# Optimization experiments

Measured on AMD Instinct MI355X. Metric: run time of the kernel, lower is better.

## Reference

```python
import jax, jax.numpy as jnp
import numpy as np

CLASS_PERIOD = 360
MEAN = True

def setup_inputs() -> dict:
    key = jax.random.key(0)
    k1, k2 = jax.random.split(key)
    preds = jax.random.normal(k1, (131072, CLASS_PERIOD), dtype=jnp.float32)
    labels = jax.random.randint(k2, (131072,), 0, CLASS_PERIOD, dtype=jnp.int64 if jax.config.jax_enable_x64 else jnp.int32)
    return {"preds": preds, "labels": labels}

def reference(preds, labels):
    # per-row L1 normalization: x_i / sum(|x_i|)
    l1 = jnp.sum(jnp.abs(preds), axis=-1, keepdims=True)        # [B, 1]
    scaled = preds / l1                                          # [B, C]
    logp = jax.nn.log_softmax(scaled, axis=-1)                   # [B, C]
    gathered = jnp.take_along_axis(logp, labels[:, None], axis=-1)[:, 0]  # [B]
    if MEAN:
        # original: (one_hot * logp).mean() per instance = logp[label] / C
        loss = -jnp.sum(gathered) / CLASS_PERIOD
    else:
        loss = -jnp.sum(gathered)
    return loss.reshape(1)
```

## Files before the change

### kernel.cpp

```cpp
#include <hip/hip_runtime.h>
#include <hip/hip_bf16.h>
#include <math.h>

#define NROWS 131072
#define NCOLS 360
#define WAVES_PER_BLOCK 4

__global__ __launch_bounds__(256) void viewpoint_row_kernel(
    const float* __restrict__ preds,
    const int* __restrict__ labels,
    float* __restrict__ partial)
{
    const int wave = threadIdx.x >> 6;
    const int lane = threadIdx.x & 63;
    const int row  = blockIdx.x * WAVES_PER_BLOCK + wave;

    const float* p = preds + (size_t)row * NCOLS;
    const float4* p4 = (const float4*)p;

    float4 a0 = p4[lane];
    float4 a1 = make_float4(0.f, 0.f, 0.f, 0.f);
    const bool have2 = lane < (90 - 64);
    if (have2) a1 = p4[64 + lane];

    float s = fabsf(a0.x) + fabsf(a0.y) + fabsf(a0.z) + fabsf(a0.w);
    float m = fmaxf(fmaxf(a0.x, a0.y), fmaxf(a0.z, a0.w));
    if (have2) {
        s += fabsf(a1.x) + fabsf(a1.y) + fabsf(a1.z) + fabsf(a1.w);
        m = fmaxf(m, fmaxf(fmaxf(a1.x, a1.y), fmaxf(a1.z, a1.w)));
    }
    #pragma unroll
    for (int off = 32; off > 0; off >>= 1) {
        s += __shfl_xor(s, off);
        m = fmaxf(m, __shfl_xor(m, off));
    }

    const float inv = 1.0f / s;

    float e = expf((a0.x - m) * inv) + expf((a0.y - m) * inv)
            + expf((a0.z - m) * inv) + expf((a0.w - m) * inv);
    if (have2) {
        e += expf((a1.x - m) * inv) + expf((a1.y - m) * inv)
           + expf((a1.z - m) * inv) + expf((a1.w - m) * inv);
    }
    #pragma unroll
    for (int off = 32; off > 0; off >>= 1) e += __shfl_xor(e, off);

    float g = 0.f;
    if (lane == 0) {
        const int lab = labels[row];
        const float xl = p[lab];
        g = (xl - m) * inv - logf(e);
    }

    __shared__ float sh[WAVES_PER_BLOCK];
    if (lane == 0) sh[wave] = g;
    __syncthreads();
    if (threadIdx.x == 0)
        partial[blockIdx.x] = sh[0] + sh[1] + sh[2] + sh[3];
}

__global__ __launch_bounds__(256) void viewpoint_final_kernel(
    const float* __restrict__ partial, float* __restrict__ out, int n)
{
    float s = 0.f;
    for (int i = threadIdx.x; i < n; i += 256) s += partial[i];
    #pragma unroll
    for (int off = 32; off > 0; off >>= 1) s += __shfl_xor(s, off);
    __shared__ float sh[4];
    if ((threadIdx.x & 63) == 0) sh[threadIdx.x >> 6] = s;
    __syncthreads();
    if (threadIdx.x == 0)
        out[0] = -(sh[0] + sh[1] + sh[2] + sh[3]) * (1.0f / (float)NCOLS);
}

extern "C" void kernel_launch(void* const* d_in, const int* in_sizes, int n_in,
                              void* d_out, int out_size, void* d_ws, size_t ws_size,
                              hipStream_t stream) {
    const float* preds  = (const float*)d_in[0];
    const int*   labels = (const int*)d_in[1];
    float* out = (float*)d_out;
    float* partial = (float*)d_ws;

    const int nblocks = NROWS / WAVES_PER_BLOCK;
    viewpoint_row_kernel<<<nblocks, 256, 0, stream>>>(preds, labels, partial);
    viewpoint_final_kernel<<<1, 256, 0, stream>>>(partial, out, nblocks);
}
```

Before: 279.8 us.

## Process eight rows per wave, drop max pass, use fast math and shuffle gather

```diff
diff --git a/kernel.cpp b/kernel.cpp
--- a/kernel.cpp
+++ b/kernel.cpp
@@ -4,7 +4,11 @@
 
 #define NROWS 131072
 #define NCOLS 360
-#define WAVES_PER_BLOCK 4
+#define ROWS_PER_WAVE 8
+#define NWAVES (NROWS / ROWS_PER_WAVE)
+#define NBLOCKS (NWAVES / 4)
+
+typedef float f32x4 __attribute__((ext_vector_type(4)));
 
 __global__ __launch_bounds__(256) void viewpoint_row_kernel(
     const float* __restrict__ preds,
@@ -13,48 +17,49 @@
 {
     const int wave = threadIdx.x >> 6;
     const int lane = threadIdx.x & 63;
-    const int row  = blockIdx.x * WAVES_PER_BLOCK + wave;
+    const int wgid = blockIdx.x * 4 + wave;
+    const bool have2 = lane < (90 - 64);
 
-    const float* p = preds + (size_t)row * NCOLS;
-    const float4* p4 = (const float4*)p;
+    float gacc = 0.f;
 
-    float4 a0 = p4[lane];
-    float4 a1 = make_float4(0.f, 0.f, 0.f, 0.f);
-    const bool have2 = lane < (90 - 64);
-    if (have2) a1 = p4[64 + lane];
+    #pragma unroll
+    for (int r = 0; r < ROWS_PER_WAVE; ++r) {
+        const int row = r * NWAVES + wgid;
+        const f32x4* p4 = (const f32x4*)(preds + (size_t)row * NCOLS);
 
-    float s = fabsf(a0.x) + fabsf(a0.y) + fabsf(a0.z) + fabsf(a0.w);
-    float m = fmaxf(fmaxf(a0.x, a0.y), fmaxf(a0.z, a0.w));
-    if (have2) {
-        s += fabsf(a1.x) + fabsf(a1.y) + fabsf(a1.z) + fabsf(a1.w);
-        m = fmaxf(m, fmaxf(fmaxf(a1.x, a1.y), fmaxf(a1.z, a1.w)));
-    }
-    #pragma unroll
-    for (int off = 32; off > 0; off >>= 1) {
-        s += __shfl_xor(s, off);
-        m = fmaxf(m, __shfl_xor(m, off));
+        f32x4 a0 = __builtin_nontemporal_load(p4 + lane);
+        f32x4 a1 = {0.f, 0.f, 0.f, 0.f};
+        if (have2) a1 = __builtin_nontemporal_load(p4 + 64 + lane);
+
+        float s = (fabsf(a0.x) + fabsf(a0.y)) + (fabsf(a0.z) + fabsf(a0.w))
+                + ((fabsf(a1.x) + fabsf(a1.y)) + (fabsf(a1.z) + fabsf(a1.w)));
+        #pragma unroll
+        for (int off = 32; off > 0; off >>= 1) s += __shfl_xor(s, off);
+
+        const float inv = __builtin_amdgcn_rcpf(s);
+
+        float e = (__expf(a0.x * inv) + __expf(a0.y * inv))
+                + (__expf(a0.z * inv) + __expf(a0.w * inv));
+        if (have2)
+            e += (__expf(a1.x * inv) + __expf(a1.y * inv))
+               + (__expf(a1.z * inv) + __expf(a1.w * inv));
+        #pragma unroll
+        for (int off = 32; off > 0; off >>= 1) e += __shfl_xor(e, off);
+
+        const int lab = labels[row];
+        const int f4i = lab >> 2;
+        const int c   = lab & 3;
+        const f32x4 src = (f4i < 64) ? a0 : a1;
+        const int owner = (f4i < 64) ? f4i : (f4i - 64);
+        const float v = (c == 0) ? src.x : (c == 1) ? src.y
+                      : (c == 2) ? src.z : src.w;
+        const float xl = __shfl(v, owner);
+
+        gacc += xl * inv - __logf(e);
     }
 
-    const float inv = 1.0f / s;
-
-    float e = expf((a0.x - m) * inv) + expf((a0.y - m) * inv)
-            + expf((a0.z - m) * inv) + expf((a0.w - m) * inv);
-    if (have2) {
-        e += expf((a1.x - m) * inv) + expf((a1.y - m) * inv)
-           + expf((a1.z - m) * inv) + expf((a1.w - m) * inv);
-    }
-    #pragma unroll
-    for (int off = 32; off > 0; off >>= 1) e += __shfl_xor(e, off);
-
-    float g = 0.f;
-    if (lane == 0) {
-        const int lab = labels[row];
-        const float xl = p[lab];
-        g = (xl - m) * inv - logf(e);
-    }
-
-    __shared__ float sh[WAVES_PER_BLOCK];
-    if (lane == 0) sh[wave] = g;
+    __shared__ float sh[4];
+    if (lane == 0) sh[wave] = gacc;
     __syncthreads();
     if (threadIdx.x == 0)
         partial[blockIdx.x] = sh[0] + sh[1] + sh[2] + sh[3];
@@ -82,7 +87,6 @@
     float* out = (float*)d_out;
     float* partial = (float*)d_ws;
 
-    const int nblocks = NROWS / WAVES_PER_BLOCK;
-    viewpoint_row_kernel<<<nblocks, 256, 0, stream>>>(preds, labels, partial);
-    viewpoint_final_kernel<<<1, 256, 0, stream>>>(partial, out, nblocks);
+    viewpoint_row_kernel<<<NBLOCKS, 256, 0, stream>>>(preds, labels, partial);
+    viewpoint_final_kernel<<<1, 256, 0, stream>>>(partial, out, NBLOCKS);
 }
```

Measured after the change: 254.4 us. 9.1% less time.
